# Optimization experiments

Hardware: AMD Instinct MI355X
Metric: run time of the kernel (lower is better)

## Reference

```python
import jax, jax.numpy as jnp
import numpy as np

B, N, M, K = 1024, 20000, 10000, 8
CHK_W, OBS_W = 8, 200          # fixed support size per check / observable row
EPS = 1e-6
BETA = 0.5


def setup_inputs() -> dict:
    rng = np.random.default_rng(0)
    # packed CSR-style support sets (fixed row weight -> dense index tables)
    chk_cols = jnp.asarray(rng.integers(0, N, size=(M, CHK_W)), dtype=jnp.int32)
    obs_cols = jnp.asarray(rng.integers(0, N, size=(K, OBS_W)), dtype=jnp.int32)
    key = jax.random.key(0)
    k1, k2, k3 = jax.random.split(key, 3)
    llrs = jax.random.normal(k1, (B, N), dtype=jnp.float32) * 2.0
    syndromes = jax.random.bernoulli(k2, 0.5, (B, M)).astype(jnp.float32)
    observables = jax.random.bernoulli(k3, 0.5, (B, K)).astype(jnp.float32)
    return {"llrs": llrs, "syndromes": syndromes, "observables": observables,
            "chk_cols": chk_cols, "obs_cols": obs_cols}


def _pred_llr(tanh_half, cols):
    # tanh_half: (B, N); cols: (R, W) -> gathered (B, R, W)
    g = tanh_half[:, cols]
    prod = jnp.prod(g, axis=-1)                       # BP check-node tanh product, (B, R)
    prod = jnp.clip(prod, -1.0 + EPS, 1.0 - EPS)
    return 2.0 * jnp.arctanh(prod)


def _bce_with_logits(z, y):
    # BCEWithLogitsLoss(z, y) = softplus(z) - z*y (numerically stable)
    return jax.nn.softplus(z) - z * y


def reference(llrs, syndromes, observables, chk_cols, obs_cols):
    t = jnp.tanh(llrs * 0.5)                          # (B, N)
    syn_pred_llr = _pred_llr(t, chk_cols)             # (B, M)
    obs_pred_llr = _pred_llr(t, obs_cols)             # (B, K)
    loss1 = _bce_with_logits(-syn_pred_llr, syndromes).sum(axis=1)
    loss2 = _bce_with_logits(-obs_pred_llr, observables).sum(axis=1)
    loss = BETA * loss1 + (1.0 - BETA) * loss2
    return loss.mean()
```

## Files before the change

kernel.cpp:

```cpp
#include <hip/hip_runtime.h>

#define B_ 1024
#define N_ 20000
#define M_ 10000
#define K_ 8
#define OBS_W_ 200
#define TPB 1024

constexpr float EPS_   = 1e-6f;
constexpr float LN2_   = 0.69314718055994530942f;
constexpr float LOG2E_ = 1.4426950408889634f;
constexpr float QSCALE   = 127.0f;
constexpr float QINV     = 1.0f / 127.0f;
constexpr float QBIASINV = -128.0f / 127.0f;

__device__ __forceinline__ float tanh_half_fast(float x) {
    float e = __builtin_amdgcn_exp2f(x * LOG2E_);
    return 1.0f - 2.0f * __builtin_amdgcn_rcpf(e + 1.0f);
}

__device__ __forceinline__ float bce_log2(float p, float y) {
    p = fminf(fmaxf(p, -1.0f + EPS_), 1.0f - EPS_);
    float w = fmaf(1.0f - 2.0f * y, p, 1.0f);
    return __builtin_amdgcn_logf(w);
}

__device__ __forceinline__ unsigned int quant8(float t) {
    return (unsigned int)(int)rintf(fmaf(t, QSCALE, 128.0f));
}
__device__ __forceinline__ unsigned int pack4_q8(float a, float b, float c, float d) {
    return quant8(a) | (quant8(b) << 8) | (quant8(c) << 16) | (quant8(d) << 24);
}
__device__ __forceinline__ float dec8(unsigned int g, int k) {
    float u = (float)((g >> (8 * k)) & 0xffu);
    return fmaf(u, QINV, QBIASINV);
}

template <bool ATOMIC>
__global__ __launch_bounds__(TPB) void decode_loss_q8(
    const float* __restrict__ llrs,
    const float* __restrict__ syndromes,
    const float* __restrict__ observables,
    const int*   __restrict__ chk_cols,
    const int*   __restrict__ obs_cols,
    float* __restrict__ part)
{
    extern __shared__ char smem_raw[];
    unsigned int* t8 = reinterpret_cast<unsigned int*>(smem_raw);
    __shared__ float red[TPB / 64];

    const int b0  = 4 * blockIdx.x;
    const int tid = threadIdx.x;

    const float4* r0 = reinterpret_cast<const float4*>(llrs + (size_t)(b0 + 0) * N_);
    const float4* r1 = reinterpret_cast<const float4*>(llrs + (size_t)(b0 + 1) * N_);
    const float4* r2 = reinterpret_cast<const float4*>(llrs + (size_t)(b0 + 2) * N_);
    const float4* r3 = reinterpret_cast<const float4*>(llrs + (size_t)(b0 + 3) * N_);
    for (int i = tid; i < N_ / 4; i += TPB) {
        float4 a = r0[i], b = r1[i], c = r2[i], d = r3[i];
        int4 w;
        w.x = (int)pack4_q8(tanh_half_fast(a.x), tanh_half_fast(b.x),
                            tanh_half_fast(c.x), tanh_half_fast(d.x));
        w.y = (int)pack4_q8(tanh_half_fast(a.y), tanh_half_fast(b.y),
                            tanh_half_fast(c.y), tanh_half_fast(d.y));
        w.z = (int)pack4_q8(tanh_half_fast(a.z), tanh_half_fast(b.z),
                            tanh_half_fast(c.z), tanh_half_fast(d.z));
        w.w = (int)pack4_q8(tanh_half_fast(a.w), tanh_half_fast(b.w),
                            tanh_half_fast(c.w), tanh_half_fast(d.w));
        *reinterpret_cast<int4*>(&t8[4 * i]) = w;
    }
    __syncthreads();

    float acc = 0.0f;
    int   cnt = 0;
    const float* syn0 = syndromes + (size_t)(b0 + 0) * M_;
    const float* syn1 = syndromes + (size_t)(b0 + 1) * M_;
    const float* syn2 = syndromes + (size_t)(b0 + 2) * M_;
    const float* syn3 = syndromes + (size_t)(b0 + 3) * M_;
    const int4*  cc   = reinterpret_cast<const int4*>(chk_cols);
    for (int m = tid; m < M_; m += TPB) {
        int4 c0 = cc[2 * m];
        int4 c1 = cc[2 * m + 1];
        unsigned int g0 = t8[c0.x], g1 = t8[c0.y], g2 = t8[c0.z], g3 = t8[c0.w];
        unsigned int g4 = t8[c1.x], g5 = t8[c1.y], g6 = t8[c1.z], g7 = t8[c1.w];
        float p0 = dec8(g0, 0), p1 = dec8(g0, 1), p2 = dec8(g0, 2), p3 = dec8(g0, 3);
        p0 *= dec8(g1, 0); p1 *= dec8(g1, 1); p2 *= dec8(g1, 2); p3 *= dec8(g1, 3);
        p0 *= dec8(g2, 0); p1 *= dec8(g2, 1); p2 *= dec8(g2, 2); p3 *= dec8(g2, 3);
        p0 *= dec8(g3, 0); p1 *= dec8(g3, 1); p2 *= dec8(g3, 2); p3 *= dec8(g3, 3);
        p0 *= dec8(g4, 0); p1 *= dec8(g4, 1); p2 *= dec8(g4, 2); p3 *= dec8(g4, 3);
        p0 *= dec8(g5, 0); p1 *= dec8(g5, 1); p2 *= dec8(g5, 2); p3 *= dec8(g5, 3);
        p0 *= dec8(g6, 0); p1 *= dec8(g6, 1); p2 *= dec8(g6, 2); p3 *= dec8(g6, 3);
        p0 *= dec8(g7, 0); p1 *= dec8(g7, 1); p2 *= dec8(g7, 2); p3 *= dec8(g7, 3);
        acc += bce_log2(p0, syn0[m]);
        acc += bce_log2(p1, syn1[m]);
        acc += bce_log2(p2, syn2[m]);
        acc += bce_log2(p3, syn3[m]);
        ++cnt;
    }
    float sum = 0.5f * LN2_ * (4.0f * (float)cnt - acc);

    if (tid < 256) {
        const int row = tid >> 6;
        const int k   = (tid >> 3) & 7;
        const int seg = tid & 7;
        const int* oc = obs_cols + k * OBS_W_ + seg * 25;
        const int sh  = 8 * row;
        float pr = 1.0f;
        #pragma unroll 5
        for (int w = 0; w < 25; ++w) {
            unsigned int gw = t8[oc[w]];
            float u = (float)((gw >> sh) & 0xffu);
            pr *= fmaf(u, QINV, QBIASINV);
        }
        #pragma unroll
        for (int off = 1; off < 8; off <<= 1) pr *= __shfl_xor(pr, off, 64);
        if (seg == 0) {
            float y = observables[(size_t)(b0 + row) * K_ + k];
            sum += 0.5f * LN2_ * (1.0f - bce_log2(pr, y));
        }
    }

    for (int off = 32; off > 0; off >>= 1) sum += __shfl_down(sum, off, 64);
    const int lane = tid & 63, wv = tid >> 6;
    if (lane == 0) red[wv] = sum;
    __syncthreads();
    if (tid == 0) {
        float tot = 0.0f;
        #pragma unroll
        for (int i = 0; i < TPB / 64; ++i) tot += red[i];
        if (ATOMIC) atomicAdd(part, tot * (1.0f / (float)B_));
        else        part[blockIdx.x] = tot;
    }
}

__global__ __launch_bounds__(256) void decode_loss_reduce(
    const float* __restrict__ part, float* __restrict__ out, int n)
{
    __shared__ float red[4];
    const int tid = threadIdx.x;
    float s = 0.0f;
    for (int i = tid; i < n; i += 256) s += part[i];
    for (int off = 32; off > 0; off >>= 1) s += __shfl_down(s, off, 64);
    const int lane = tid & 63, wv = tid >> 6;
    if (lane == 0) red[wv] = s;
    __syncthreads();
    if (tid == 0) out[0] = (red[0] + red[1] + red[2] + red[3]) * (1.0f / (float)B_);
}

extern "C" void kernel_launch(void* const* d_in, const int* in_sizes, int n_in,
                              void* d_out, int out_size, void* d_ws, size_t ws_size,
                              hipStream_t stream) {
    const float* llrs        = (const float*)d_in[0];
    const float* syndromes   = (const float*)d_in[1];
    const float* observables = (const float*)d_in[2];
    const int*   chk_cols    = (const int*)d_in[3];
    const int*   obs_cols    = (const int*)d_in[4];
    float*       out         = (float*)d_out;

    const size_t lds_bytes = (size_t)N_ * 4;
    const int    nblk      = B_ / 4;

    (void)hipFuncSetAttribute((const void*)decode_loss_q8<false>,
        hipFuncAttributeMaxDynamicSharedMemorySize, (int)lds_bytes);
    (void)hipFuncSetAttribute((const void*)decode_loss_q8<true>,
        hipFuncAttributeMaxDynamicSharedMemorySize, (int)lds_bytes);

    if (ws_size >= (size_t)nblk * sizeof(float)) {
        float* part = (float*)d_ws;
        decode_loss_q8<false><<<nblk, TPB, lds_bytes, stream>>>(
            llrs, syndromes, observables, chk_cols, obs_cols, part);
        decode_loss_reduce<<<1, 256, 0, stream>>>(part, out, nblk);
    } else {
        hipMemsetAsync(out, 0, sizeof(float), stream);
        decode_loss_q8<true><<<nblk, TPB, lds_bytes, stream>>>(
            llrs, syndromes, observables, chk_cols, obs_cols, out);
    }
}
```

Before: 29.43 us.

## Switch tanh table to fp16 pairs and overlap second half's load with checks

Replaces the 8-bit quantized 4-row tanh table with two fp16x2 tables, each holding two batch rows. Loads and converts rows 2-3 while the check products for rows 0-1 are computed, so global loads overlap with LDS gathers. The products now use packed half-precision multiplies instead of per-byte decode. LDS use doubles to 160KB and there are two gather passes instead of one, which may cut occupancy and add LDS traffic. fp16 products over 8 terms may lose precision near the clip bounds.

```diff
diff --git a/kernel.cpp b/kernel.cpp
--- a/kernel.cpp
+++ b/kernel.cpp
@@ -6,13 +6,14 @@
 #define K_ 8
 #define OBS_W_ 200
 #define TPB 1024
+#define NV4 (N_ / 4)
 
 constexpr float EPS_   = 1e-6f;
 constexpr float LN2_   = 0.69314718055994530942f;
 constexpr float LOG2E_ = 1.4426950408889634f;
-constexpr float QSCALE   = 127.0f;
-constexpr float QINV     = 1.0f / 127.0f;
-constexpr float QBIASINV = -128.0f / 127.0f;
+
+typedef _Float16 f16x2 __attribute__((ext_vector_type(2)));
+typedef _Float16 f16x8 __attribute__((ext_vector_type(8)));
 
 __device__ __forceinline__ float tanh_half_fast(float x) {
     float e = __builtin_amdgcn_exp2f(x * LOG2E_);
@@ -25,19 +26,32 @@
     return __builtin_amdgcn_logf(w);
 }
 
-__device__ __forceinline__ unsigned int quant8(float t) {
-    return (unsigned int)(int)rintf(fmaf(t, QSCALE, 128.0f));
+__device__ __forceinline__ void do_check2(const f16x2* __restrict__ t2,
+                                          const float* __restrict__ synA,
+                                          const float* __restrict__ synB,
+                                          const int4* __restrict__ cc,
+                                          int m, float& acc, int& nterm) {
+    int4 c0 = cc[2 * m];
+    int4 c1 = cc[2 * m + 1];
+    f16x2 g0 = t2[c0.x], g1 = t2[c0.y], g2 = t2[c0.z], g3 = t2[c0.w];
+    f16x2 g4 = t2[c1.x], g5 = t2[c1.y], g6 = t2[c1.z], g7 = t2[c1.w];
+    f16x2 p  = ((g0 * g1) * (g2 * g3)) * ((g4 * g5) * (g6 * g7));
+    acc += bce_log2((float)p[0], synA[m]);
+    acc += bce_log2((float)p[1], synB[m]);
+    nterm += 2;
 }
-__device__ __forceinline__ unsigned int pack4_q8(float a, float b, float c, float d) {
-    return quant8(a) | (quant8(b) << 8) | (quant8(c) << 16) | (quant8(d) << 24);
-}
-__device__ __forceinline__ float dec8(unsigned int g, int k) {
-    float u = (float)((g >> (8 * k)) & 0xffu);
-    return fmaf(u, QINV, QBIASINV);
+
+__device__ __forceinline__ f16x8 pack2(float4 a, float4 c) {
+    f16x8 v;
+    v[0] = (_Float16)tanh_half_fast(a.x); v[1] = (_Float16)tanh_half_fast(c.x);
+    v[2] = (_Float16)tanh_half_fast(a.y); v[3] = (_Float16)tanh_half_fast(c.y);
+    v[4] = (_Float16)tanh_half_fast(a.z); v[5] = (_Float16)tanh_half_fast(c.z);
+    v[6] = (_Float16)tanh_half_fast(a.w); v[7] = (_Float16)tanh_half_fast(c.w);
+    return v;
 }
 
 template <bool ATOMIC>
-__global__ __launch_bounds__(TPB) void decode_loss_q8(
+__global__ __launch_bounds__(TPB) void decode_loss_pipe(
     const float* __restrict__ llrs,
     const float* __restrict__ syndromes,
     const float* __restrict__ observables,
@@ -46,7 +60,8 @@
     float* __restrict__ part)
 {
     extern __shared__ char smem_raw[];
-    unsigned int* t8 = reinterpret_cast<unsigned int*>(smem_raw);
+    f16x2* t2a = reinterpret_cast<f16x2*>(smem_raw);
+    f16x2* t2b = t2a + N_;
     __shared__ float red[TPB / 64];
 
     const int b0  = 4 * blockIdx.x;
@@ -56,62 +71,51 @@
     const float4* r1 = reinterpret_cast<const float4*>(llrs + (size_t)(b0 + 1) * N_);
     const float4* r2 = reinterpret_cast<const float4*>(llrs + (size_t)(b0 + 2) * N_);
     const float4* r3 = reinterpret_cast<const float4*>(llrs + (size_t)(b0 + 3) * N_);
-    for (int i = tid; i < N_ / 4; i += TPB) {
-        float4 a = r0[i], b = r1[i], c = r2[i], d = r3[i];
-        int4 w;
-        w.x = (int)pack4_q8(tanh_half_fast(a.x), tanh_half_fast(b.x),
-                            tanh_half_fast(c.x), tanh_half_fast(d.x));
-        w.y = (int)pack4_q8(tanh_half_fast(a.y), tanh_half_fast(b.y),
-                            tanh_half_fast(c.y), tanh_half_fast(d.y));
-        w.z = (int)pack4_q8(tanh_half_fast(a.z), tanh_half_fast(b.z),
-                            tanh_half_fast(c.z), tanh_half_fast(d.z));
-        w.w = (int)pack4_q8(tanh_half_fast(a.w), tanh_half_fast(b.w),
-                            tanh_half_fast(c.w), tanh_half_fast(d.w));
-        *reinterpret_cast<int4*>(&t8[4 * i]) = w;
+
+    for (int i = tid; i < NV4; i += TPB) {
+        *reinterpret_cast<f16x8*>(&t2a[4 * i]) = pack2(r0[i], r1[i]);
     }
     __syncthreads();
 
-    float acc = 0.0f;
-    int   cnt = 0;
     const float* syn0 = syndromes + (size_t)(b0 + 0) * M_;
     const float* syn1 = syndromes + (size_t)(b0 + 1) * M_;
     const float* syn2 = syndromes + (size_t)(b0 + 2) * M_;
     const float* syn3 = syndromes + (size_t)(b0 + 3) * M_;
     const int4*  cc   = reinterpret_cast<const int4*>(chk_cols);
+
+    float acc   = 0.0f;
+    int   nterm = 0;
+
+    #pragma unroll 1
+    for (int it = 0; it < 5; ++it) {
+        const int  i  = tid + it * TPB;
+        const bool iv = (i < NV4);
+        float4 a, c;
+        if (iv) { a = r2[i]; c = r3[i]; }
+        const int m0 = tid + (2 * it) * TPB;
+        const int m1 = m0 + TPB;
+        if (m0 < M_) do_check2(t2a, syn0, syn1, cc, m0, acc, nterm);
+        if (m1 < M_) do_check2(t2a, syn0, syn1, cc, m1, acc, nterm);
+        if (iv) *reinterpret_cast<f16x8*>(&t2b[4 * i]) = pack2(a, c);
+    }
+    __syncthreads();
+
     for (int m = tid; m < M_; m += TPB) {
-        int4 c0 = cc[2 * m];
-        int4 c1 = cc[2 * m + 1];
-        unsigned int g0 = t8[c0.x], g1 = t8[c0.y], g2 = t8[c0.z], g3 = t8[c0.w];
-        unsigned int g4 = t8[c1.x], g5 = t8[c1.y], g6 = t8[c1.z], g7 = t8[c1.w];
-        float p0 = dec8(g0, 0), p1 = dec8(g0, 1), p2 = dec8(g0, 2), p3 = dec8(g0, 3);
-        p0 *= dec8(g1, 0); p1 *= dec8(g1, 1); p2 *= dec8(g1, 2); p3 *= dec8(g1, 3);
-        p0 *= dec8(g2, 0); p1 *= dec8(g2, 1); p2 *= dec8(g2, 2); p3 *= dec8(g2, 3);
-        p0 *= dec8(g3, 0); p1 *= dec8(g3, 1); p2 *= dec8(g3, 2); p3 *= dec8(g3, 3);
-        p0 *= dec8(g4, 0); p1 *= dec8(g4, 1); p2 *= dec8(g4, 2); p3 *= dec8(g4, 3);
-        p0 *= dec8(g5, 0); p1 *= dec8(g5, 1); p2 *= dec8(g5, 2); p3 *= dec8(g5, 3);
-        p0 *= dec8(g6, 0); p1 *= dec8(g6, 1); p2 *= dec8(g6, 2); p3 *= dec8(g6, 3);
-        p0 *= dec8(g7, 0); p1 *= dec8(g7, 1); p2 *= dec8(g7, 2); p3 *= dec8(g7, 3);
-        acc += bce_log2(p0, syn0[m]);
-        acc += bce_log2(p1, syn1[m]);
-        acc += bce_log2(p2, syn2[m]);
-        acc += bce_log2(p3, syn3[m]);
-        ++cnt;
+        do_check2(t2b, syn2, syn3, cc, m, acc, nterm);
     }
-    float sum = 0.5f * LN2_ * (4.0f * (float)cnt - acc);
+
+    float sum = 0.5f * LN2_ * ((float)nterm - acc);
 
     if (tid < 256) {
-        const int row = tid >> 6;
-        const int k   = (tid >> 3) & 7;
-        const int seg = tid & 7;
-        const int* oc = obs_cols + k * OBS_W_ + seg * 25;
-        const int sh  = 8 * row;
+        const int row  = tid >> 6;
+        const int k    = (tid >> 3) & 7;
+        const int seg  = tid & 7;
+        const f16x2* tb   = (row < 2) ? t2a : t2b;
+        const int    comp = row & 1;
+        const int*   oc   = obs_cols + k * OBS_W_ + seg * 25;
         float pr = 1.0f;
         #pragma unroll 5
-        for (int w = 0; w < 25; ++w) {
-            unsigned int gw = t8[oc[w]];
-            float u = (float)((gw >> sh) & 0xffu);
-            pr *= fmaf(u, QINV, QBIASINV);
-        }
+        for (int w = 0; w < 25; ++w) pr *= (float)tb[oc[w]][comp];
         #pragma unroll
         for (int off = 1; off < 8; off <<= 1) pr *= __shfl_xor(pr, off, 64);
         if (seg == 0) {
@@ -157,22 +161,22 @@
     const int*   obs_cols    = (const int*)d_in[4];
     float*       out         = (float*)d_out;
 
-    const size_t lds_bytes = (size_t)N_ * 4;
+    const size_t lds_bytes = (size_t)N_ * 2 * sizeof(f16x2);
     const int    nblk      = B_ / 4;
 
-    (void)hipFuncSetAttribute((const void*)decode_loss_q8<false>,
+    (void)hipFuncSetAttribute((const void*)decode_loss_pipe<false>,
         hipFuncAttributeMaxDynamicSharedMemorySize, (int)lds_bytes);
-    (void)hipFuncSetAttribute((const void*)decode_loss_q8<true>,
+    (void)hipFuncSetAttribute((const void*)decode_loss_pipe<true>,
         hipFuncAttributeMaxDynamicSharedMemorySize, (int)lds_bytes);
 
     if (ws_size >= (size_t)nblk * sizeof(float)) {
         float* part = (float*)d_ws;
-        decode_loss_q8<false><<<nblk, TPB, lds_bytes, stream>>>(
+        decode_loss_pipe<false><<<nblk, TPB, lds_bytes, stream>>>(
             llrs, syndromes, observables, chk_cols, obs_cols, part);
         decode_loss_reduce<<<1, 256, 0, stream>>>(part, out, nblk);
     } else {
         hipMemsetAsync(out, 0, sizeof(float), stream);
-        decode_loss_q8<true><<<nblk, TPB, lds_bytes, stream>>>(
+        decode_loss_pipe<true><<<nblk, TPB, lds_bytes, stream>>>(
             llrs, syndromes, observables, chk_cols, obs_cols, out);
     }
 }
```

After: 29.23 us. Within noise of the previous version (-0.7%).

## Store tanh table as packed fp16 and multiply gathered values in half precision

Applied to the files above, without the earlier changes.

Replaces the 8-bit quantized tanh table in LDS with an fp16x4 table, so each gather returns four batch rows as half values. The 8-way check product is computed with packed fp16 vector multiplies instead of per-element byte decode and fp32 multiplies. The four BCE log terms are merged into a single log of a product. LDS usage doubles to 160 KB per block and each gather moves 8 bytes instead of 4, trading higher LDS bandwidth for fewer ALU decode instructions and fewer log calls. Precision shifts from 8-bit quantization to fp16, with some risk of underflow in the product.

```diff
diff --git a/kernel.cpp b/kernel.cpp
--- a/kernel.cpp
+++ b/kernel.cpp
@@ -10,34 +10,21 @@
 constexpr float EPS_   = 1e-6f;
 constexpr float LN2_   = 0.69314718055994530942f;
 constexpr float LOG2E_ = 1.4426950408889634f;
-constexpr float QSCALE   = 127.0f;
-constexpr float QINV     = 1.0f / 127.0f;
-constexpr float QBIASINV = -128.0f / 127.0f;
+
+typedef _Float16 f16x4 __attribute__((ext_vector_type(4)));
+typedef _Float16 f16x8 __attribute__((ext_vector_type(8)));
 
 __device__ __forceinline__ float tanh_half_fast(float x) {
     float e = __builtin_amdgcn_exp2f(x * LOG2E_);
     return 1.0f - 2.0f * __builtin_amdgcn_rcpf(e + 1.0f);
 }
 
-__device__ __forceinline__ float bce_log2(float p, float y) {
-    p = fminf(fmaxf(p, -1.0f + EPS_), 1.0f - EPS_);
-    float w = fmaf(1.0f - 2.0f * y, p, 1.0f);
-    return __builtin_amdgcn_logf(w);
-}
-
-__device__ __forceinline__ unsigned int quant8(float t) {
-    return (unsigned int)(int)rintf(fmaf(t, QSCALE, 128.0f));
-}
-__device__ __forceinline__ unsigned int pack4_q8(float a, float b, float c, float d) {
-    return quant8(a) | (quant8(b) << 8) | (quant8(c) << 16) | (quant8(d) << 24);
-}
-__device__ __forceinline__ float dec8(unsigned int g, int k) {
-    float u = (float)((g >> (8 * k)) & 0xffu);
-    return fmaf(u, QINV, QBIASINV);
+__device__ __forceinline__ float clampp(float p) {
+    return fminf(fmaxf(p, -1.0f + EPS_), 1.0f - EPS_);
 }
 
 template <bool ATOMIC>
-__global__ __launch_bounds__(TPB) void decode_loss_q8(
+__global__ __launch_bounds__(TPB) void decode_loss_m4(
     const float* __restrict__ llrs,
     const float* __restrict__ syndromes,
     const float* __restrict__ observables,
@@ -46,7 +33,7 @@
     float* __restrict__ part)
 {
     extern __shared__ char smem_raw[];
-    unsigned int* t8 = reinterpret_cast<unsigned int*>(smem_raw);
+    f16x4* t4 = reinterpret_cast<f16x4*>(smem_raw);
     __shared__ float red[TPB / 64];
 
     const int b0  = 4 * blockIdx.x;
@@ -58,16 +45,17 @@
     const float4* r3 = reinterpret_cast<const float4*>(llrs + (size_t)(b0 + 3) * N_);
     for (int i = tid; i < N_ / 4; i += TPB) {
         float4 a = r0[i], b = r1[i], c = r2[i], d = r3[i];
-        int4 w;
-        w.x = (int)pack4_q8(tanh_half_fast(a.x), tanh_half_fast(b.x),
-                            tanh_half_fast(c.x), tanh_half_fast(d.x));
-        w.y = (int)pack4_q8(tanh_half_fast(a.y), tanh_half_fast(b.y),
-                            tanh_half_fast(c.y), tanh_half_fast(d.y));
-        w.z = (int)pack4_q8(tanh_half_fast(a.z), tanh_half_fast(b.z),
-                            tanh_half_fast(c.z), tanh_half_fast(d.z));
-        w.w = (int)pack4_q8(tanh_half_fast(a.w), tanh_half_fast(b.w),
-                            tanh_half_fast(c.w), tanh_half_fast(d.w));
-        *reinterpret_cast<int4*>(&t8[4 * i]) = w;
+        f16x8 w01, w23;
+        w01[0] = (_Float16)tanh_half_fast(a.x); w01[1] = (_Float16)tanh_half_fast(b.x);
+        w01[2] = (_Float16)tanh_half_fast(c.x); w01[3] = (_Float16)tanh_half_fast(d.x);
+        w01[4] = (_Float16)tanh_half_fast(a.y); w01[5] = (_Float16)tanh_half_fast(b.y);
+        w01[6] = (_Float16)tanh_half_fast(c.y); w01[7] = (_Float16)tanh_half_fast(d.y);
+        w23[0] = (_Float16)tanh_half_fast(a.z); w23[1] = (_Float16)tanh_half_fast(b.z);
+        w23[2] = (_Float16)tanh_half_fast(c.z); w23[3] = (_Float16)tanh_half_fast(d.z);
+        w23[4] = (_Float16)tanh_half_fast(a.w); w23[5] = (_Float16)tanh_half_fast(b.w);
+        w23[6] = (_Float16)tanh_half_fast(c.w); w23[7] = (_Float16)tanh_half_fast(d.w);
+        *reinterpret_cast<f16x8*>(&t4[4 * i + 0]) = w01;
+        *reinterpret_cast<f16x8*>(&t4[4 * i + 2]) = w23;
     }
     __syncthreads();
 
@@ -81,48 +69,38 @@
     for (int m = tid; m < M_; m += TPB) {
         int4 c0 = cc[2 * m];
         int4 c1 = cc[2 * m + 1];
-        unsigned int g0 = t8[c0.x], g1 = t8[c0.y], g2 = t8[c0.z], g3 = t8[c0.w];
-        unsigned int g4 = t8[c1.x], g5 = t8[c1.y], g6 = t8[c1.z], g7 = t8[c1.w];
-        float p0 = dec8(g0, 0), p1 = dec8(g0, 1), p2 = dec8(g0, 2), p3 = dec8(g0, 3);
-        p0 *= dec8(g1, 0); p1 *= dec8(g1, 1); p2 *= dec8(g1, 2); p3 *= dec8(g1, 3);
-        p0 *= dec8(g2, 0); p1 *= dec8(g2, 1); p2 *= dec8(g2, 2); p3 *= dec8(g2, 3);
-        p0 *= dec8(g3, 0); p1 *= dec8(g3, 1); p2 *= dec8(g3, 2); p3 *= dec8(g3, 3);
-        p0 *= dec8(g4, 0); p1 *= dec8(g4, 1); p2 *= dec8(g4, 2); p3 *= dec8(g4, 3);
-        p0 *= dec8(g5, 0); p1 *= dec8(g5, 1); p2 *= dec8(g5, 2); p3 *= dec8(g5, 3);
-        p0 *= dec8(g6, 0); p1 *= dec8(g6, 1); p2 *= dec8(g6, 2); p3 *= dec8(g6, 3);
-        p0 *= dec8(g7, 0); p1 *= dec8(g7, 1); p2 *= dec8(g7, 2); p3 *= dec8(g7, 3);
-        acc += bce_log2(p0, syn0[m]);
-        acc += bce_log2(p1, syn1[m]);
-        acc += bce_log2(p2, syn2[m]);
-        acc += bce_log2(p3, syn3[m]);
-        ++cnt;
+        f16x4 g0 = t4[c0.x], g1 = t4[c0.y], g2 = t4[c0.z], g3 = t4[c0.w];
+        f16x4 g4 = t4[c1.x], g5 = t4[c1.y], g6 = t4[c1.z], g7 = t4[c1.w];
+        f16x4 p  = ((g0 * g1) * (g2 * g3)) * ((g4 * g5) * (g6 * g7));
+        float w0 = fmaf(fmaf(syn0[m], -2.0f, 1.0f), clampp((float)p[0]), 1.0f);
+        float w1 = fmaf(fmaf(syn1[m], -2.0f, 1.0f), clampp((float)p[1]), 1.0f);
+        float w2 = fmaf(fmaf(syn2[m], -2.0f, 1.0f), clampp((float)p[2]), 1.0f);
+        float w3 = fmaf(fmaf(syn3[m], -2.0f, 1.0f), clampp((float)p[3]), 1.0f);
+        acc += __builtin_amdgcn_logf((w0 * w1) * (w2 * w3));
+        cnt += 4;
     }
-    float sum = 0.5f * LN2_ * (4.0f * (float)cnt - acc);
+    float sum = 0.5f * LN2_ * ((float)cnt - acc);
 
     if (tid < 256) {
         const int row = tid >> 6;
         const int k   = (tid >> 3) & 7;
         const int seg = tid & 7;
         const int* oc = obs_cols + k * OBS_W_ + seg * 25;
-        const int sh  = 8 * row;
         float pr = 1.0f;
         #pragma unroll 5
-        for (int w = 0; w < 25; ++w) {
-            unsigned int gw = t8[oc[w]];
-            float u = (float)((gw >> sh) & 0xffu);
-            pr *= fmaf(u, QINV, QBIASINV);
-        }
+        for (int w = 0; w < 25; ++w) { f16x4 gg = t4[oc[w]]; pr *= (float)gg[row]; }
         #pragma unroll
         for (int off = 1; off < 8; off <<= 1) pr *= __shfl_xor(pr, off, 64);
         if (seg == 0) {
-            float y = observables[(size_t)(b0 + row) * K_ + k];
-            sum += 0.5f * LN2_ * (1.0f - bce_log2(pr, y));
+            float y  = observables[(size_t)(b0 + row) * K_ + k];
+            float wv = fmaf(fmaf(y, -2.0f, 1.0f), clampp(pr), 1.0f);
+            sum += 0.5f * LN2_ * (1.0f - __builtin_amdgcn_logf(wv));
         }
     }
 
     for (int off = 32; off > 0; off >>= 1) sum += __shfl_down(sum, off, 64);
-    const int lane = tid & 63, wv = tid >> 6;
-    if (lane == 0) red[wv] = sum;
+    const int lane = tid & 63, wv2 = tid >> 6;
+    if (lane == 0) red[wv2] = sum;
     __syncthreads();
     if (tid == 0) {
         float tot = 0.0f;
@@ -157,22 +135,22 @@
     const int*   obs_cols    = (const int*)d_in[4];
     float*       out         = (float*)d_out;
 
-    const size_t lds_bytes = (size_t)N_ * 4;
+    const size_t lds_bytes = (size_t)N_ * 8;
     const int    nblk      = B_ / 4;
 
-    (void)hipFuncSetAttribute((const void*)decode_loss_q8<false>,
+    (void)hipFuncSetAttribute((const void*)decode_loss_m4<false>,
         hipFuncAttributeMaxDynamicSharedMemorySize, (int)lds_bytes);
-    (void)hipFuncSetAttribute((const void*)decode_loss_q8<true>,
+    (void)hipFuncSetAttribute((const void*)decode_loss_m4<true>,
         hipFuncAttributeMaxDynamicSharedMemorySize, (int)lds_bytes);
 
     if (ws_size >= (size_t)nblk * sizeof(float)) {
         float* part = (float*)d_ws;
-        decode_loss_q8<false><<<nblk, TPB, lds_bytes, stream>>>(
+        decode_loss_m4<false><<<nblk, TPB, lds_bytes, stream>>>(
             llrs, syndromes, observables, chk_cols, obs_cols, part);
         decode_loss_reduce<<<1, 256, 0, stream>>>(part, out, nblk);
     } else {
         hipMemsetAsync(out, 0, sizeof(float), stream);
-        decode_loss_q8<true><<<nblk, TPB, lds_bytes, stream>>>(
+        decode_loss_m4<true><<<nblk, TPB, lds_bytes, stream>>>(
             llrs, syndromes, observables, chk_cols, obs_cols, out);
     }
 }
```

Result: faster. 26.46 us (-10.1%).
